# Performance work log

Measured on AMD Instinct MI355X. Metric: run time of the kernel, lower is better.

The kernel has to match this reference:

```python
import jax, jax.numpy as jnp
import numpy as np

EPS = 1e-5  # torch InstanceNorm1d default

def _inorm(x):
    # instance norm over length dim per (batch, channel), no affine, biased var
    m = jnp.mean(x, axis=-1, keepdims=True)
    v = jnp.var(x, axis=-1, keepdims=True)
    return (x - m) * jax.lax.rsqrt(v + EPS)

def _conv1x1(W, b, x):
    # kernel-size-1 Conv1d == per-position linear: [O,C] x [B,C,T] -> [B,O,T]
    return jnp.einsum('oc,bct->bot', W, x) + b[None, :, None]

def setup_inputs() -> dict:
    key = jax.random.key(0)
    ks = jax.random.split(key, 10)
    B, C, T = 4, 512, 2048
    s = 1.0 / np.sqrt(C)  # conv1d default init scale
    return {
        'x_c': jax.random.normal(ks[0], (B, C, T), jnp.float32),
        'x_s': jax.random.normal(ks[1], (B, C, T), jnp.float32),
        'Wn': jax.random.normal(ks[2], (C, C), jnp.float32) * s,
        'bn': jax.random.normal(ks[3], (C,), jnp.float32) * s,
        'Wm': jax.random.normal(ks[4], (C, C), jnp.float32) * s,
        'bm': jax.random.normal(ks[5], (C,), jnp.float32) * s,
        'Wl': jax.random.normal(ks[6], (C, C), jnp.float32) * s,
        'bl': jax.random.normal(ks[7], (C,), jnp.float32) * s,
        'Wo': jax.random.normal(ks[8], (C, C), jnp.float32) * s,
        'bo': jax.random.normal(ks[9], (C,), jnp.float32) * s,
    }

def reference(x_c, x_s, Wn, bn, Wm, bm, Wl, bl, Wo, bo):
    Mn = _conv1x1(Wn, bn, _inorm(x_c))           # [B,C,Tc]
    Mm = _conv1x1(Wm, bm, _inorm(x_s))           # [B,C,Ts]
    A = jax.nn.softmax(jnp.einsum('bct,bcs->bts', Mn, Mm), axis=-1)  # [B,Tc,Ts]
    Ml = _conv1x1(Wl, bl, x_s)                   # [B,C,Ts]
    Mo = jnp.einsum('bcs,bts->bct', Ml, A)       # [B,C,Tc]
    return _conv1x1(Wo, bo, Mo) + x_c
```

## Files before the change

### kernel.cpp

```cpp
#include <hip/hip_runtime.h>
#include <hip/hip_bf16.h>
#include <stdint.h>

typedef _Float16 f16;
typedef _Float16 f16x8 __attribute__((ext_vector_type(8)));
typedef _Float16 f16x4 __attribute__((ext_vector_type(4)));
typedef float    f32x4 __attribute__((ext_vector_type(4)));

#define BB 4
#define CC 512
#define TT 2048

__device__ __forceinline__ void gload16(const void* g, void* l) {
  __builtin_amdgcn_global_load_lds((const __attribute__((address_space(1))) void*)g,
                                   (__attribute__((address_space(3))) void*)l, 16, 0, 0);
}

template <int N>
__device__ __forceinline__ void s_wait_vmcnt() {
  if constexpr (N == 0)      asm volatile("s_waitcnt vmcnt(0)" ::: "memory");
  else if constexpr (N == 4) asm volatile("s_waitcnt vmcnt(4)" ::: "memory");
  else if constexpr (N == 6) asm volatile("s_waitcnt vmcnt(6)" ::: "memory");
}

__device__ __forceinline__ void xcd_swizzle(int& bx, int& by, int& bz) {
  int gx = gridDim.x, gy = gridDim.y;
  int F = bx + gx * (by + gy * bz);
  int q = (gx * gy * gridDim.z) >> 3;
  int l = (F & 7) * q + (F >> 3);
  bx = l % gx; by = (l / gx) % gy; bz = l / (gx * gy);
}

__global__ __launch_bounds__(256) void transpose_kernel(
    const float* __restrict__ xc, const float* __restrict__ xs,
    f16* __restrict__ xcT, f16* __restrict__ xsT,
    float* __restrict__ sumc, float* __restrict__ sqc,
    float* __restrict__ sums_, float* __restrict__ sqs) {
  const int b = blockIdx.z & 3, which = blockIdx.z >> 2;
  const float* src = (which ? xs : xc) + (long)b * CC * TT;
  f16* dst = (which ? xsT : xcT) + (long)b * TT * CC;
  float* sumP = (which ? sums_ : sumc) + b * CC;
  float* sqP  = (which ? sqs   : sqc ) + b * CC;
  const int t0 = blockIdx.x * 64, c0 = blockIdx.y * 64;
  __shared__ float tile[64][65];
  const int tid = threadIdx.x;
  #pragma unroll
  for (int it = 0; it < 4; ++it) {
    int s = it * 256 + tid, r = s >> 4, q = s & 15;
    float4 v = *(const float4*)&src[(long)(c0 + r) * TT + t0 + q * 4];
    tile[r][q*4+0] = v.x; tile[r][q*4+1] = v.y; tile[r][q*4+2] = v.z; tile[r][q*4+3] = v.w;
    float ps = v.x + v.y + v.z + v.w;
    float pq = v.x*v.x + v.y*v.y + v.z*v.z + v.w*v.w;
    #pragma unroll
    for (int o = 8; o; o >>= 1) { ps += __shfl_xor(ps, o); pq += __shfl_xor(pq, o); }
    if ((tid & 15) == 0) {
      atomicAdd(&sumP[c0 + r], ps);
      atomicAdd(&sqP [c0 + r], pq);
    }
  }
  __syncthreads();
  #pragma unroll
  for (int it = 0; it < 4; ++it) {
    int s = it * 256 + tid, r = s >> 4, q = s & 15;
    f16x4 o;
    o[0] = (f16)tile[q*4+0][r]; o[1] = (f16)tile[q*4+1][r];
    o[2] = (f16)tile[q*4+2][r]; o[3] = (f16)tile[q*4+3][r];
    *(f16x4*)&dst[(long)(t0 + r) * CC + c0 + q * 4] = o;
  }
}

__global__ __launch_bounds__(256) void prepw_kernel(
    const float* __restrict__ W, const float* __restrict__ bias,
    const float* __restrict__ sum, const float* __restrict__ sq,
    f16* __restrict__ Weff, float* __restrict__ beff) {
  const int o = blockIdx.x, b = blockIdx.y, tid = threadIdx.x;
  float acc = 0.f;
  #pragma unroll
  for (int j = 0; j < 2; ++j) {
    int c = tid + j * 256;
    float mean = sum[b * CC + c] * (1.f / TT);
    float var  = sq [b * CC + c] * (1.f / TT) - mean * mean;
    float iv = 1.0f / sqrtf(var + 1e-5f);
    float wv = W[(long)o * CC + c] * iv;
    Weff[((long)b * CC + o) * CC + c] = (f16)wv;
    acc += wv * mean;
  }
  #pragma unroll
  for (int off = 32; off; off >>= 1) acc += __shfl_xor(acc, off);
  __shared__ float red[4];
  if ((tid & 63) == 0) red[tid >> 6] = acc;
  __syncthreads();
  if (tid == 0) beff[b * CC + o] = bias[o] - (red[0] + red[1] + red[2] + red[3]);
}

__global__ __launch_bounds__(256) void f2h_kernel(const float* __restrict__ src,
                                                  f16* __restrict__ dst) {
  long i = ((long)blockIdx.x * 256 + threadIdx.x) * 8;
  float4 a = *(const float4*)&src[i], d = *(const float4*)&src[i + 4];
  f16x8 o;
  o[0]=(f16)a.x; o[1]=(f16)a.y; o[2]=(f16)a.z; o[3]=(f16)a.w;
  o[4]=(f16)d.x; o[5]=(f16)d.y; o[6]=(f16)d.z; o[7]=(f16)d.w;
  *(f16x8*)&dst[i] = o;
}

__global__ __launch_bounds__(256) void softmax_kernel(f16* __restrict__ S) {
  f16* p = S + ((long)blockIdx.y * TT + blockIdx.x) * TT;
  const int tid = threadIdx.x;
  f16x8 v8 = ((const f16x8*)p)[tid];
  float v[8];
  #pragma unroll
  for (int j = 0; j < 8; ++j) v[j] = (float)v8[j];
  float m = v[0];
  #pragma unroll
  for (int j = 1; j < 8; ++j) m = fmaxf(m, v[j]);
  #pragma unroll
  for (int o = 32; o; o >>= 1) m = fmaxf(m, __shfl_xor(m, o));
  __shared__ float red[4], red2[4];
  if (!(tid & 63)) red[tid >> 6] = m;
  __syncthreads();
  m = fmaxf(fmaxf(red[0], red[1]), fmaxf(red[2], red[3]));
  float e[8], sum = 0.f;
  #pragma unroll
  for (int j = 0; j < 8; ++j) { e[j] = __expf(v[j] - m); sum += e[j]; }
  #pragma unroll
  for (int o = 32; o; o >>= 1) sum += __shfl_xor(sum, o);
  if (!(tid & 63)) red2[tid >> 6] = sum;
  __syncthreads();
  sum = red2[0] + red2[1] + red2[2] + red2[3];
  float is = 1.f / sum;
  f16x8 o8;
  #pragma unroll
  for (int j = 0; j < 8; ++j) o8[j] = (f16)(e[j] * is);
  ((f16x8*)p)[tid] = o8;
}

template <int BM, int NT, typename OutT>
__device__ __forceinline__ void gemm_core(
    const f16* __restrict__ A, int lda,
    const f16* __restrict__ BT, int ldb,
    OutT* __restrict__ C, int ldc,
    const float* __restrict__ bias,
    const float* __restrict__ resid, int ldres,
    int bm, int bn, int K, bool transw) {

  constexpr int CA = BM * 8 / NT;
  constexpr int CB = 128 * 8 / NT;
  constexpr int LOADS = CA + CB;
  constexpr int ABUFB = BM * 128;
  constexpr int BBUFB = 128 * 128;

  __shared__ f16 sA[3 * BM * 64];
  __shared__ f16 sB[3 * 128 * 64];

  const int tid = threadIdx.x, lane = tid & 63, wv = tid >> 6;
  const int wr = wv >> 1, wc = wv & 1;

  const char* gAp[CA]; int lAo[CA];
  #pragma unroll
  for (int i = 0; i < CA; ++i) {
    int cid = tid + i * NT, row = cid >> 3;
    int colb = ((cid & 7) * 16) ^ ((row & 7) << 4);
    gAp[i] = (const char*)A + (long)(bm + row) * lda * 2 + colb;
    lAo[i] = cid * 16;
  }
  const char* gBp[CB]; int lBo[CB];
  #pragma unroll
  for (int i = 0; i < CB; ++i) {
    int cid = tid + i * NT, row = cid >> 3;
    int colb = ((cid & 7) * 16) ^ ((row & 7) << 4);
    gBp[i] = (const char*)BT + (long)(bn + row) * ldb * 2 + colb;
    lBo[i] = cid * 16;
  }

  const int lm = lane & 15, lkb = (lane >> 4) * 16, sw = (lane & 7) << 4;
  int aoff[2][2], boff[4][2];
  #pragma unroll
  for (int mi = 0; mi < 2; ++mi) {
    int r = wr * 32 + mi * 16 + lm;
    #pragma unroll
    for (int kk = 0; kk < 2; ++kk)
      aoff[mi][kk] = r * 128 + ((kk * 64 + lkb) ^ sw);
  }
  #pragma unroll
  for (int ni = 0; ni < 4; ++ni) {
    int r = wc * 64 + ni * 16 + lm;
    #pragma unroll
    for (int kk = 0; kk < 2; ++kk)
      boff[ni][kk] = r * 128 + ((kk * 64 + lkb) ^ sw);
  }

  f32x4 acc[2][4] = {};
  const int nk = K >> 6;

  #pragma unroll
  for (int i = 0; i < CA; ++i) gload16(gAp[i], (char*)sA + lAo[i]);
  #pragma unroll
  for (int i = 0; i < CB; ++i) gload16(gBp[i], (char*)sB + lBo[i]);
  #pragma unroll
  for (int i = 0; i < CA; ++i) gload16(gAp[i] + 128, (char*)sA + ABUFB + lAo[i]);
  #pragma unroll
  for (int i = 0; i < CB; ++i) gload16(gBp[i] + 128, (char*)sB + BBUFB + lBo[i]);

  int s0 = 0;
  for (int kt = 0; kt < nk; ++kt) {
    if (kt + 1 < nk) s_wait_vmcnt<LOADS>(); else s_wait_vmcnt<0>();
    __builtin_amdgcn_s_barrier();

    if (kt + 2 < nk) {
      int s2 = s0 + 2; if (s2 >= 3) s2 -= 3;
      long kb = (long)(kt + 2) * 128;
      int na = s2 * ABUFB, nb = s2 * BBUFB;
      #pragma unroll
      for (int i = 0; i < CA; ++i) gload16(gAp[i] + kb, (char*)sA + na + lAo[i]);
      #pragma unroll
      for (int i = 0; i < CB; ++i) gload16(gBp[i] + kb, (char*)sB + nb + lBo[i]);
    }

    const char* pa = (const char*)sA + s0 * ABUFB;
    const char* pb = (const char*)sB + s0 * BBUFB;
    f16x8 af[2][2], bf[4][2];
    #pragma unroll
    for (int mi = 0; mi < 2; ++mi)
      #pragma unroll
      for (int kk = 0; kk < 2; ++kk)
        af[mi][kk] = *(const f16x8*)(pa + aoff[mi][kk]);
    #pragma unroll
    for (int ni = 0; ni < 4; ++ni)
      #pragma unroll
      for (int kk = 0; kk < 2; ++kk)
        bf[ni][kk] = *(const f16x8*)(pb + boff[ni][kk]);
    #pragma unroll
    for (int kk = 0; kk < 2; ++kk)
      #pragma unroll
      for (int mi = 0; mi < 2; ++mi)
        #pragma unroll
        for (int ni = 0; ni < 4; ++ni)
          acc[mi][ni] = __builtin_amdgcn_mfma_f32_16x16x32_f16(af[mi][kk], bf[ni][kk], acc[mi][ni], 0, 0, 0);

    __builtin_amdgcn_s_barrier();
    s0 = (s0 == 2) ? 0 : s0 + 1;
  }

  struct alignas(4 * sizeof(OutT)) Pack4 { OutT v[4]; };
  const int rr = (lane >> 4) * 4;
  #pragma unroll
  for (int mi = 0; mi < 2; ++mi) {
    int m0 = bm + wr * 32 + mi * 16 + rr;
    #pragma unroll
    for (int ni = 0; ni < 4; ++ni) {
      int n0 = bn + wc * 64 + ni * 16 + lm;
      f32x4 v = acc[mi][ni];
      float vals[4];
      #pragma unroll
      for (int r = 0; r < 4; ++r) {
        vals[r] = v[r];
        if (bias)  vals[r] += bias[m0 + r];
        if (resid) vals[r] += resid[(long)(m0 + r) * ldres + n0];
      }
      if (transw) {
        Pack4 pk;
        #pragma unroll
        for (int r = 0; r < 4; ++r) pk.v[r] = (OutT)vals[r];
        *(Pack4*)&C[(long)n0 * ldc + m0] = pk;
      } else {
        #pragma unroll
        for (int r = 0; r < 4; ++r)
          C[(long)(m0 + r) * ldc + n0] = (OutT)vals[r];
      }
    }
  }
}

__global__ __launch_bounds__(512) void conv_kernel(
    const f16* __restrict__ xcT, const f16* __restrict__ xsT,
    const f16* __restrict__ WnE, const float* __restrict__ bnE,
    const f16* __restrict__ WmE, const float* __restrict__ bmE,
    const f16* __restrict__ WlB, const float* __restrict__ bl,
    f16* __restrict__ MnT, f16* __restrict__ MmT, f16* __restrict__ Ml) {
  int bx = blockIdx.x, by = blockIdx.y, bz = blockIdx.z;
  xcd_swizzle(bx, by, bz);
  const int cid = bz >> 2, b = bz & 3;
  const f16* A; const float* bias; const f16* B; f16* C; int ldc; bool transw;
  if (cid == 0)      { A = WnE + (long)b*CC*CC; bias = bnE + b*CC; B = xcT + (long)b*TT*CC; C = MnT + (long)b*TT*CC; ldc = CC; transw = true; }
  else if (cid == 1) { A = WmE + (long)b*CC*CC; bias = bmE + b*CC; B = xsT + (long)b*TT*CC; C = MmT + (long)b*TT*CC; ldc = CC; transw = true; }
  else               { A = WlB;                 bias = bl;         B = xsT + (long)b*TT*CC; C = Ml  + (long)b*CC*TT; ldc = TT; transw = false; }
  gemm_core<128, 512, f16>(A, CC, B, CC, C, ldc, bias, nullptr, 0,
                           by * 128, bx * 128, CC, transw);
}

__global__ __launch_bounds__(512) void sgemm_kernel(
    const f16* __restrict__ MnT, const f16* __restrict__ MmT, f16* __restrict__ S) {
  int bx = blockIdx.x, by = blockIdx.y, bz = blockIdx.z;
  xcd_swizzle(bx, by, bz);
  gemm_core<128, 512, f16>(MnT + (long)bz*TT*CC, CC, MmT + (long)bz*TT*CC, CC,
                           S + (long)bz*TT*TT, TT, nullptr, nullptr, 0,
                           by * 128, bx * 128, CC, false);
}

__global__ __launch_bounds__(256) void pv_kernel(
    const f16* __restrict__ P, const f16* __restrict__ Ml, f16* __restrict__ MoT) {
  int bx = blockIdx.x, by = blockIdx.y, bz = blockIdx.z;
  xcd_swizzle(bx, by, bz);
  gemm_core<64, 256, f16>(P + (long)bz*TT*TT, TT, Ml + (long)bz*CC*TT, TT,
                          MoT + (long)bz*TT*CC, CC, nullptr, nullptr, 0,
                          by * 64, bx * 128, TT, false);
}

__global__ __launch_bounds__(256) void out_kernel(
    const f16* __restrict__ WoB, const f16* __restrict__ MoT,
    const float* __restrict__ bo, const float* __restrict__ xc, float* __restrict__ out) {
  int bx = blockIdx.x, by = blockIdx.y, bz = blockIdx.z;
  xcd_swizzle(bx, by, bz);
  gemm_core<64, 256, float>(WoB, CC, MoT + (long)bz*TT*CC, CC,
                            out + (long)bz*CC*TT, TT, bo, xc + (long)bz*CC*TT, TT,
                            by * 64, bx * 128, CC, false);
}

extern "C" void kernel_launch(void* const* d_in, const int* in_sizes, int n_in,
                              void* d_out, int out_size, void* d_ws, size_t ws_size,
                              hipStream_t stream) {
  const float* x_c = (const float*)d_in[0];
  const float* x_s = (const float*)d_in[1];
  const float* Wn  = (const float*)d_in[2];
  const float* bn  = (const float*)d_in[3];
  const float* Wm  = (const float*)d_in[4];
  const float* bm  = (const float*)d_in[5];
  const float* Wl  = (const float*)d_in[6];
  const float* bl  = (const float*)d_in[7];
  const float* Wo  = (const float*)d_in[8];
  const float* bo  = (const float*)d_in[9];
  float* out = (float*)d_out;

  char* w = (char*)d_ws;
  auto alloc = [&](size_t bytes) { char* p = w; w += (bytes + 255) & ~(size_t)255; return p; };
  float* sumc = (float*)alloc(BB * CC * 4);
  float* sqc  = (float*)alloc(BB * CC * 4);
  float* sums_ = (float*)alloc(BB * CC * 4);
  float* sqs  = (float*)alloc(BB * CC * 4);
  float* bnE  = (float*)alloc(BB * CC * 4);
  float* bmE  = (float*)alloc(BB * CC * 4);
  f16* WnE = (f16*)alloc((size_t)BB * CC * CC * 2);
  f16* WmE = (f16*)alloc((size_t)BB * CC * CC * 2);
  f16* WlB = (f16*)alloc((size_t)CC * CC * 2);
  f16* WoB = (f16*)alloc((size_t)CC * CC * 2);
  f16* xcT = (f16*)alloc((size_t)BB * TT * CC * 2);
  f16* xsT = (f16*)alloc((size_t)BB * TT * CC * 2);
  f16* MnT = (f16*)alloc((size_t)BB * TT * CC * 2);
  f16* MmT = (f16*)alloc((size_t)BB * TT * CC * 2);
  f16* Ml  = (f16*)alloc((size_t)BB * CC * TT * 2);
  f16* S   = (f16*)alloc((size_t)BB * TT * TT * 2);
  f16* MoT = (f16*)alloc((size_t)BB * TT * CC * 2);

  hipMemsetAsync(sumc, 0, (size_t)4 * BB * CC * 4, stream);

  transpose_kernel<<<dim3(TT / 64, CC / 64, BB * 2), dim3(256), 0, stream>>>(
      x_c, x_s, xcT, xsT, sumc, sqc, sums_, sqs);
  prepw_kernel<<<dim3(CC, BB), dim3(256), 0, stream>>>(Wn, bn, sumc, sqc, WnE, bnE);
  prepw_kernel<<<dim3(CC, BB), dim3(256), 0, stream>>>(Wm, bm, sums_, sqs, WmE, bmE);
  f2h_kernel<<<dim3(CC * CC / (256 * 8)), dim3(256), 0, stream>>>(Wl, WlB);
  f2h_kernel<<<dim3(CC * CC / (256 * 8)), dim3(256), 0, stream>>>(Wo, WoB);

  conv_kernel<<<dim3(16, 4, 12), dim3(512), 0, stream>>>(
      xcT, xsT, WnE, bnE, WmE, bmE, WlB, bl, MnT, MmT, Ml);
  sgemm_kernel<<<dim3(16, 16, BB), dim3(512), 0, stream>>>(MnT, MmT, S);
  softmax_kernel<<<dim3(TT, BB), dim3(256), 0, stream>>>(S);
  pv_kernel<<<dim3(4, 32, BB), dim3(256), 0, stream>>>(S, Ml, MoT);
  out_kernel<<<dim3(16, 8, BB), dim3(256), 0, stream>>>(WoB, MoT, bo, x_c, out);
}
```

Measured before the change: 227.0 us.

## Fuse softmax into score GEMM stats and PV GEMM prologue, merge prep launches

Removes the standalone softmax pass over the score matrix. The score GEMM now emits per-tile row max and exp-sum partials, and a small kernel merges them into a per-row max and inverse sum. The PV GEMM is rewritten with a 256x64 tile that loads raw scores through registers, applies exp(s - max) before the LDS store, and scales by the inverse sum in the epilogue. The two prepw launches and the two f2h launches are each merged into one launch. The PV GEMM now evaluates exp once per element for every column tile, since it recomputes them redundantly across the 8 column blocks, and A loads move from async LDS DMA to register staging.

```diff
diff --git a/kernel.cpp b/kernel.cpp
--- a/kernel.cpp
+++ b/kernel.cpp
@@ -70,10 +70,19 @@
 }
 
 __global__ __launch_bounds__(256) void prepw_kernel(
-    const float* __restrict__ W, const float* __restrict__ bias,
-    const float* __restrict__ sum, const float* __restrict__ sq,
-    f16* __restrict__ Weff, float* __restrict__ beff) {
-  const int o = blockIdx.x, b = blockIdx.y, tid = threadIdx.x;
+    const float* __restrict__ Wn, const float* __restrict__ bn,
+    const float* __restrict__ Wm, const float* __restrict__ bm_,
+    const float* __restrict__ sumc, const float* __restrict__ sqc,
+    const float* __restrict__ sums_, const float* __restrict__ sqs,
+    f16* __restrict__ WnE, float* __restrict__ bnE,
+    f16* __restrict__ WmE, float* __restrict__ bmE) {
+  const int o = blockIdx.x, b = blockIdx.y, which = blockIdx.z, tid = threadIdx.x;
+  const float* W    = which ? Wm : Wn;
+  const float* bias = which ? bm_ : bn;
+  const float* sum  = which ? sums_ : sumc;
+  const float* sq   = which ? sqs : sqc;
+  f16* Weff   = which ? WmE : WnE;
+  float* beff = which ? bmE : bnE;
   float acc = 0.f;
   #pragma unroll
   for (int j = 0; j < 2; ++j) {
@@ -93,8 +102,12 @@
   if (tid == 0) beff[b * CC + o] = bias[o] - (red[0] + red[1] + red[2] + red[3]);
 }
 
-__global__ __launch_bounds__(256) void f2h_kernel(const float* __restrict__ src,
-                                                  f16* __restrict__ dst) {
+__global__ __launch_bounds__(256) void f2h_kernel(const float* __restrict__ s0,
+                                                  f16* __restrict__ d0,
+                                                  const float* __restrict__ s1,
+                                                  f16* __restrict__ d1) {
+  const float* src = blockIdx.y ? s1 : s0;
+  f16* dst = blockIdx.y ? d1 : d0;
   long i = ((long)blockIdx.x * 256 + threadIdx.x) * 8;
   float4 a = *(const float4*)&src[i], d = *(const float4*)&src[i + 4];
   f16x8 o;
@@ -103,45 +116,35 @@
   *(f16x8*)&dst[i] = o;
 }
 
-__global__ __launch_bounds__(256) void softmax_kernel(f16* __restrict__ S) {
-  f16* p = S + ((long)blockIdx.y * TT + blockIdx.x) * TT;
-  const int tid = threadIdx.x;
-  f16x8 v8 = ((const f16x8*)p)[tid];
-  float v[8];
-  #pragma unroll
-  for (int j = 0; j < 8; ++j) v[j] = (float)v8[j];
-  float m = v[0];
-  #pragma unroll
-  for (int j = 1; j < 8; ++j) m = fmaxf(m, v[j]);
-  #pragma unroll
-  for (int o = 32; o; o >>= 1) m = fmaxf(m, __shfl_xor(m, o));
-  __shared__ float red[4], red2[4];
-  if (!(tid & 63)) red[tid >> 6] = m;
-  __syncthreads();
-  m = fmaxf(fmaxf(red[0], red[1]), fmaxf(red[2], red[3]));
-  float e[8], sum = 0.f;
-  #pragma unroll
-  for (int j = 0; j < 8; ++j) { e[j] = __expf(v[j] - m); sum += e[j]; }
-  #pragma unroll
-  for (int o = 32; o; o >>= 1) sum += __shfl_xor(sum, o);
-  if (!(tid & 63)) red2[tid >> 6] = sum;
-  __syncthreads();
-  sum = red2[0] + red2[1] + red2[2] + red2[3];
-  float is = 1.f / sum;
-  f16x8 o8;
-  #pragma unroll
-  for (int j = 0; j < 8; ++j) o8[j] = (f16)(e[j] * is);
-  ((f16x8*)p)[tid] = o8;
-}
-
-template <int BM, int NT, typename OutT>
+__global__ __launch_bounds__(256) void statmerge_kernel(
+    const float* __restrict__ gmP, const float* __restrict__ gsP,
+    float* __restrict__ m_out, float* __restrict__ inv_out) {
+  int idx = blockIdx.x * 256 + threadIdx.x;
+  int b = idx >> 11, t = idx & (TT - 1);
+  float mi[16];
+  float M = -3.4e38f;
+  #pragma unroll
+  for (int i = 0; i < 16; ++i) {
+    mi[i] = gmP[((long)i * BB + b) * TT + t];
+    M = fmaxf(M, mi[i]);
+  }
+  float s = 0.f;
+  #pragma unroll
+  for (int i = 0; i < 16; ++i)
+    s += gsP[((long)i * BB + b) * TT + t] * __expf(mi[i] - M);
+  m_out[idx] = M;
+  inv_out[idx] = 1.0f / s;
+}
+
+template <int BM, int NT, typename OutT, bool STATS>
 __device__ __forceinline__ void gemm_core(
     const f16* __restrict__ A, int lda,
     const f16* __restrict__ BT, int ldb,
     OutT* __restrict__ C, int ldc,
     const float* __restrict__ bias,
     const float* __restrict__ resid, int ldres,
-    int bm, int bn, int K, bool transw) {
+    int bm, int bn, int K, bool transw,
+    float* __restrict__ smaxg, float* __restrict__ ssumg) {
 
   constexpr int CA = BM * 8 / NT;
   constexpr int CB = 128 * 8 / NT;
@@ -239,6 +242,41 @@
 
     __builtin_amdgcn_s_barrier();
     s0 = (s0 == 2) ? 0 : s0 + 1;
+  }
+
+  if constexpr (STATS) {
+    __shared__ float s_mx[2][128];
+    __shared__ float s_sm[2][128];
+    #pragma unroll
+    for (int mi = 0; mi < 2; ++mi) {
+      #pragma unroll
+      for (int r = 0; r < 4; ++r) {
+        float sv[4];
+        #pragma unroll
+        for (int ni = 0; ni < 4; ++ni) sv[ni] = (float)(f16)acc[mi][ni][r];
+        float mx = sv[0];
+        #pragma unroll
+        for (int ni = 1; ni < 4; ++ni) mx = fmaxf(mx, sv[ni]);
+        #pragma unroll
+        for (int o = 1; o < 16; o <<= 1) mx = fmaxf(mx, __shfl_xor(mx, o));
+        float se = 0.f;
+        #pragma unroll
+        for (int ni = 0; ni < 4; ++ni) se += __expf(sv[ni] - mx);
+        #pragma unroll
+        for (int o = 1; o < 16; o <<= 1) se += __shfl_xor(se, o);
+        if (lm == 0) {
+          int row = wr * 32 + mi * 16 + (lane >> 4) * 4 + r;
+          s_mx[wc][row] = mx; s_sm[wc][row] = se;
+        }
+      }
+    }
+    __syncthreads();
+    if (tid < 128) {
+      float m0 = s_mx[0][tid], m1 = s_mx[1][tid];
+      float M = fmaxf(m0, m1);
+      float Ss = s_sm[0][tid] * __expf(m0 - M) + s_sm[1][tid] * __expf(m1 - M);
+      smaxg[tid] = M; ssumg[tid] = Ss;
+    }
   }
 
   struct alignas(4 * sizeof(OutT)) Pack4 { OutT v[4]; };
@@ -284,26 +322,154 @@
   if (cid == 0)      { A = WnE + (long)b*CC*CC; bias = bnE + b*CC; B = xcT + (long)b*TT*CC; C = MnT + (long)b*TT*CC; ldc = CC; transw = true; }
   else if (cid == 1) { A = WmE + (long)b*CC*CC; bias = bmE + b*CC; B = xsT + (long)b*TT*CC; C = MmT + (long)b*TT*CC; ldc = CC; transw = true; }
   else               { A = WlB;                 bias = bl;         B = xsT + (long)b*TT*CC; C = Ml  + (long)b*CC*TT; ldc = TT; transw = false; }
-  gemm_core<128, 512, f16>(A, CC, B, CC, C, ldc, bias, nullptr, 0,
-                           by * 128, bx * 128, CC, transw);
+  gemm_core<128, 512, f16, false>(A, CC, B, CC, C, ldc, bias, nullptr, 0,
+                                  by * 128, bx * 128, CC, transw, nullptr, nullptr);
 }
 
 __global__ __launch_bounds__(512) void sgemm_kernel(
-    const f16* __restrict__ MnT, const f16* __restrict__ MmT, f16* __restrict__ S) {
+    const f16* __restrict__ MnT, const f16* __restrict__ MmT, f16* __restrict__ S,
+    float* __restrict__ gmP, float* __restrict__ gsP) {
   int bx = blockIdx.x, by = blockIdx.y, bz = blockIdx.z;
   xcd_swizzle(bx, by, bz);
-  gemm_core<128, 512, f16>(MnT + (long)bz*TT*CC, CC, MmT + (long)bz*TT*CC, CC,
-                           S + (long)bz*TT*TT, TT, nullptr, nullptr, 0,
-                           by * 128, bx * 128, CC, false);
-}
-
-__global__ __launch_bounds__(256) void pv_kernel(
-    const f16* __restrict__ P, const f16* __restrict__ Ml, f16* __restrict__ MoT) {
+  float* smaxg = gmP + ((long)bx * BB + bz) * TT + by * 128;
+  float* ssumg = gsP + ((long)bx * BB + bz) * TT + by * 128;
+  gemm_core<128, 512, f16, true>(MnT + (long)bz*TT*CC, CC, MmT + (long)bz*TT*CC, CC,
+                                 S + (long)bz*TT*TT, TT, nullptr, nullptr, 0,
+                                 by * 128, bx * 128, CC, false, smaxg, ssumg);
+}
+
+__global__ __launch_bounds__(512) void pv_kernel(
+    const f16* __restrict__ Sg, const f16* __restrict__ Ml,
+    const float* __restrict__ gm, const float* __restrict__ ginv,
+    f16* __restrict__ MoT) {
   int bx = blockIdx.x, by = blockIdx.y, bz = blockIdx.z;
   xcd_swizzle(bx, by, bz);
-  gemm_core<64, 256, f16>(P + (long)bz*TT*TT, TT, Ml + (long)bz*CC*TT, TT,
-                          MoT + (long)bz*TT*CC, CC, nullptr, nullptr, 0,
-                          by * 64, bx * 128, TT, false);
+  const f16* A  = Sg + (long)bz * TT * TT;
+  const f16* BT = Ml + (long)bz * CC * TT;
+  const float* mrow = gm  + bz * TT;
+  const float* irow = ginv + bz * TT;
+  f16* C = MoT + (long)bz * TT * CC;
+  const int bm = by * 256, bn = bx * 64;
+
+  constexpr int ABUFB = 256 * 128;
+  constexpr int BBUFB = 64 * 128;
+  __shared__ f16 sA[3 * 256 * 64];
+  __shared__ f16 sB[3 * 64 * 64];
+
+  const int tid = threadIdx.x, lane = tid & 63, wv = tid >> 6;
+
+  const char* gAp[4]; int aw[4]; float am[4];
+  #pragma unroll
+  for (int i = 0; i < 4; ++i) {
+    int cid = tid + i * 512, row = cid >> 3;
+    gAp[i] = (const char*)(A + (long)(bm + row) * TT + (cid & 7) * 8);
+    aw[i] = row * 128 + (((cid & 7) * 16) ^ ((row & 7) << 4));
+    am[i] = mrow[bm + row];
+  }
+  const int brow = tid >> 3;
+  const char* gBp = (const char*)BT + (long)(bn + brow) * TT * 2 + (((tid & 7) * 16) ^ ((brow & 7) << 4));
+  char* lB = (char*)sB + tid * 16;
+
+  const int lm = lane & 15, lkb = (lane >> 4) * 16, sw = (lane & 7) << 4;
+  int aoff[2][2], boff[4][2];
+  #pragma unroll
+  for (int mi = 0; mi < 2; ++mi) {
+    int r = wv * 32 + mi * 16 + lm;
+    #pragma unroll
+    for (int kk = 0; kk < 2; ++kk)
+      aoff[mi][kk] = r * 128 + ((kk * 64 + lkb) ^ sw);
+  }
+  #pragma unroll
+  for (int ni = 0; ni < 4; ++ni) {
+    int r = ni * 16 + lm;
+    #pragma unroll
+    for (int kk = 0; kk < 2; ++kk)
+      boff[ni][kk] = r * 128 + ((kk * 64 + lkb) ^ sw);
+  }
+
+  f32x4 acc[2][4] = {};
+  const int nk = TT >> 6;
+
+  gload16(gBp, lB);
+  gload16(gBp + 128, lB + BBUFB);
+  f16x8 ar[4];
+  #pragma unroll
+  for (int i = 0; i < 4; ++i) ar[i] = *(const f16x8*)gAp[i];
+  #pragma unroll
+  for (int i = 0; i < 4; ++i) {
+    f16x8 v = ar[i]; f16x8 o;
+    #pragma unroll
+    for (int j = 0; j < 8; ++j) o[j] = (f16)__expf((float)v[j] - am[i]);
+    *(f16x8*)((char*)sA + aw[i]) = o;
+  }
+  #pragma unroll
+  for (int i = 0; i < 4; ++i) ar[i] = *(const f16x8*)(gAp[i] + 128);
+  asm volatile("s_waitcnt lgkmcnt(0)" ::: "memory");
+  __builtin_amdgcn_s_barrier();
+
+  for (int kt = 0; kt < nk; ++kt) {
+    const int s0 = kt % 3;
+    if (kt + 2 < nk)
+      gload16(gBp + (long)(kt + 2) * 128, lB + ((kt + 2) % 3) * BBUFB);
+
+    const char* pa = (const char*)sA + s0 * ABUFB;
+    const char* pb = (const char*)sB + s0 * BBUFB;
+    f16x8 af[2][2], bf[4][2];
+    #pragma unroll
+    for (int mi = 0; mi < 2; ++mi)
+      #pragma unroll
+      for (int kk = 0; kk < 2; ++kk)
+        af[mi][kk] = *(const f16x8*)(pa + aoff[mi][kk]);
+    #pragma unroll
+    for (int ni = 0; ni < 4; ++ni)
+      #pragma unroll
+      for (int kk = 0; kk < 2; ++kk)
+        bf[ni][kk] = *(const f16x8*)(pb + boff[ni][kk]);
+    #pragma unroll
+    for (int kk = 0; kk < 2; ++kk)
+      #pragma unroll
+      for (int mi = 0; mi < 2; ++mi)
+        #pragma unroll
+        for (int ni = 0; ni < 4; ++ni)
+          acc[mi][ni] = __builtin_amdgcn_mfma_f32_16x16x32_f16(af[mi][kk], bf[ni][kk], acc[mi][ni], 0, 0, 0);
+
+    if (kt + 1 < nk) {
+      const int s1b = ((kt + 1) % 3) * ABUFB;
+      #pragma unroll
+      for (int i = 0; i < 4; ++i) {
+        f16x8 v = ar[i]; f16x8 o;
+        #pragma unroll
+        for (int j = 0; j < 8; ++j) o[j] = (f16)__expf((float)v[j] - am[i]);
+        *(f16x8*)((char*)sA + s1b + aw[i]) = o;
+      }
+      if (kt + 2 < nk) {
+        #pragma unroll
+        for (int i = 0; i < 4; ++i) ar[i] = *(const f16x8*)(gAp[i] + (long)(kt + 2) * 128);
+      }
+    }
+    asm volatile("s_waitcnt lgkmcnt(0)" ::: "memory");
+    __builtin_amdgcn_s_barrier();
+  }
+
+  const int rr = (lane >> 4) * 4;
+  float iv[2][4];
+  #pragma unroll
+  for (int mi = 0; mi < 2; ++mi)
+    #pragma unroll
+    for (int r = 0; r < 4; ++r)
+      iv[mi][r] = irow[bm + wv * 32 + mi * 16 + rr + r];
+  #pragma unroll
+  for (int mi = 0; mi < 2; ++mi) {
+    int m0 = bm + wv * 32 + mi * 16 + rr;
+    #pragma unroll
+    for (int ni = 0; ni < 4; ++ni) {
+      int n0 = bn + ni * 16 + lm;
+      f32x4 v = acc[mi][ni];
+      #pragma unroll
+      for (int r = 0; r < 4; ++r)
+        C[(long)(m0 + r) * CC + n0] = (f16)(v[r] * iv[mi][r]);
+    }
+  }
 }
 
 __global__ __launch_bounds__(256) void out_kernel(
@@ -311,9 +477,9 @@
     const float* __restrict__ bo, const float* __restrict__ xc, float* __restrict__ out) {
   int bx = blockIdx.x, by = blockIdx.y, bz = blockIdx.z;
   xcd_swizzle(bx, by, bz);
-  gemm_core<64, 256, float>(WoB, CC, MoT + (long)bz*TT*CC, CC,
-                            out + (long)bz*CC*TT, TT, bo, xc + (long)bz*CC*TT, TT,
-                            by * 64, bx * 128, CC, false);
+  gemm_core<64, 256, float, false>(WoB, CC, MoT + (long)bz*TT*CC, CC,
+                                   out + (long)bz*CC*TT, TT, bo, xc + (long)bz*CC*TT, TT,
+                                   by * 64, bx * 128, CC, false, nullptr, nullptr);
 }
 
 extern "C" void kernel_launch(void* const* d_in, const int* in_sizes, int n_in,
@@ -333,12 +499,12 @@
 
   char* w = (char*)d_ws;
   auto alloc = [&](size_t bytes) { char* p = w; w += (bytes + 255) & ~(size_t)255; return p; };
-  float* sumc = (float*)alloc(BB * CC * 4);
-  float* sqc  = (float*)alloc(BB * CC * 4);
+  float* sumc  = (float*)alloc(BB * CC * 4);
+  float* sqc   = (float*)alloc(BB * CC * 4);
   float* sums_ = (float*)alloc(BB * CC * 4);
-  float* sqs  = (float*)alloc(BB * CC * 4);
-  float* bnE  = (float*)alloc(BB * CC * 4);
-  float* bmE  = (float*)alloc(BB * CC * 4);
+  float* sqs   = (float*)alloc(BB * CC * 4);
+  float* bnE   = (float*)alloc(BB * CC * 4);
+  float* bmE   = (float*)alloc(BB * CC * 4);
   f16* WnE = (f16*)alloc((size_t)BB * CC * CC * 2);
   f16* WmE = (f16*)alloc((size_t)BB * CC * CC * 2);
   f16* WlB = (f16*)alloc((size_t)CC * CC * 2);
@@ -350,20 +516,23 @@
   f16* Ml  = (f16*)alloc((size_t)BB * CC * TT * 2);
   f16* S   = (f16*)alloc((size_t)BB * TT * TT * 2);
   f16* MoT = (f16*)alloc((size_t)BB * TT * CC * 2);
+  float* gmP = (float*)alloc((size_t)16 * BB * TT * 4);
+  float* gsP = (float*)alloc((size_t)16 * BB * TT * 4);
+  float* gM  = (float*)alloc((size_t)BB * TT * 4);
+  float* gInv= (float*)alloc((size_t)BB * TT * 4);
 
   hipMemsetAsync(sumc, 0, (size_t)4 * BB * CC * 4, stream);
 
   transpose_kernel<<<dim3(TT / 64, CC / 64, BB * 2), dim3(256), 0, stream>>>(
       x_c, x_s, xcT, xsT, sumc, sqc, sums_, sqs);
-  prepw_kernel<<<dim3(CC, BB), dim3(256), 0, stream>>>(Wn, bn, sumc, sqc, WnE, bnE);
-  prepw_kernel<<<dim3(CC, BB), dim3(256), 0, stream>>>(Wm, bm, sums_, sqs, WmE, bmE);
-  f2h_kernel<<<dim3(CC * CC / (256 * 8)), dim3(256), 0, stream>>>(Wl, WlB);
-  f2h_kernel<<<dim3(CC * CC / (256 * 8)), dim3(256), 0, stream>>>(Wo, WoB);
+  prepw_kernel<<<dim3(CC, BB, 2), dim3(256), 0, stream>>>(
+      Wn, bn, Wm, bm, sumc, sqc, sums_, sqs, WnE, bnE, WmE, bmE);
+  f2h_kernel<<<dim3(CC * CC / (256 * 8), 2), dim3(256), 0, stream>>>(Wl, WlB, Wo, WoB);
 
   conv_kernel<<<dim3(16, 4, 12), dim3(512), 0, stream>>>(
       xcT, xsT, WnE, bnE, WmE, bmE, WlB, bl, MnT, MmT, Ml);
-  sgemm_kernel<<<dim3(16, 16, BB), dim3(512), 0, stream>>>(MnT, MmT, S);
-  softmax_kernel<<<dim3(TT, BB), dim3(256), 0, stream>>>(S);
-  pv_kernel<<<dim3(4, 32, BB), dim3(256), 0, stream>>>(S, Ml, MoT);
+  sgemm_kernel<<<dim3(16, 16, BB), dim3(512), 0, stream>>>(MnT, MmT, S, gmP, gsP);
+  statmerge_kernel<<<dim3(BB * TT / 256), dim3(256), 0, stream>>>(gmP, gsP, gM, gInv);
+  pv_kernel<<<dim3(8, 8, BB), dim3(512), 0, stream>>>(S, Ml, gM, gInv, MoT);
   out_kernel<<<dim3(16, 8, BB), dim3(256), 0, stream>>>(WoB, MoT, bo, x_c, out);
 }
```

Measured after the change: 250.0 us. +10.1%, slower.
